# Kernel optimization log

Measured on AMD Instinct MI355X. Metric: run time of the kernel, lower is better.

Reference implementation:

```python
import jax, jax.numpy as jnp
import numpy as np

B, T, U, L, C = 2048, 100, 512, 3, 10


def setup_inputs() -> dict:
    key = jax.random.key(0)
    ks = jax.random.split(key, 2 + 3 * L + 2)
    x = jax.random.normal(ks[0], (B, T, 1), dtype=jnp.float32)
    mask = jax.random.randint(ks[1], (B, T), 0, 2) > 0
    inp = {"x": x, "mask": mask}
    in_dim = 1
    s = 2
    for l in range(L):
        # Keras LSTM kernel layout: gates ordered [i, f, g(candidate), o]
        inp[f"W{l}"] = jax.random.normal(ks[s], (in_dim, 4 * U), dtype=jnp.float32) * 0.05
        inp[f"U{l}"] = jax.random.normal(ks[s + 1], (U, 4 * U), dtype=jnp.float32) * 0.05
        b = np.zeros((4 * U,), dtype=np.float32)
        b[U:2 * U] = 1.0  # unit_forget_bias (Keras default)
        inp[f"b{l}"] = jnp.asarray(b)
        in_dim = U
        s += 2
    inp["Wd"] = jax.random.normal(ks[s], (U, C), dtype=jnp.float32) * 0.05
    inp["bd"] = jnp.zeros((C,), dtype=jnp.float32)
    return inp


def _lstm_step(x_t, h, c, W, Uw, b):
    z = x_t @ W + h @ Uw + b  # [B, 4U]
    i, f, g, o = jnp.split(z, 4, axis=-1)
    i = jax.nn.sigmoid(i)
    f = jax.nn.sigmoid(f)
    g = jnp.tanh(g)
    o = jax.nn.sigmoid(o)
    c_new = f * c + i * g
    h_new = o * jnp.tanh(c_new)
    return h_new, c_new


def reference(x, mask, W0, U0, b0, W1, U1, b1, W2, U2, b2, Wd, bd):
    params = [(W0, U0, b0), (W1, U1, b1), (W2, U2, b2)]
    xt = jnp.swapaxes(x, 0, 1)        # [T, B, 1]
    mt = jnp.swapaxes(mask, 0, 1)     # [T, B]
    Bsz = x.shape[0]
    init = tuple((jnp.zeros((Bsz, U), x.dtype), jnp.zeros((Bsz, U), x.dtype)) for _ in range(L))

    def scan_fn(carry, inp_t):
        x_t, m_t = inp_t
        m = m_t[:, None]  # [B, 1]
        new_states = []
        layer_in = x_t
        for (h, c), (W, Uw, b) in zip(carry, params):
            h_new, c_new = _lstm_step(layer_in, h, c, W, Uw, b)
            # Keras mask semantics: masked steps carry state/output forward
            h_new = jnp.where(m, h_new, h)
            c_new = jnp.where(m, c_new, c)
            new_states.append((h_new, c_new))
            layer_in = h_new
        return tuple(new_states), None

    final, _ = jax.lax.scan(scan_fn, init, (xt, mt))
    h_top = final[-1][0]  # [B, U]
    logits = h_top @ Wd + bd
    return jax.nn.softmax(logits, axis=-1)
```

## Files before the change

### kernel.cpp

```cpp
#include <hip/hip_runtime.h>
#include <cstdint>
#include <cstddef>

#define B_   2048
#define T_   100
#define U_   512
#define NG_  2048
#define C_   10

typedef __attribute__((ext_vector_type(8))) short   short8;
typedef __attribute__((ext_vector_type(4))) float   floatx4;
typedef unsigned short ushort_t;

__device__ inline ushort_t f2bf(float f){
  unsigned u = __float_as_uint(f);
  unsigned r = (u + 0x7FFFu + ((u >> 16) & 1u)) >> 16;
  return (ushort_t)r;
}
__device__ inline float bf2f(ushort_t b){ return __uint_as_float(((unsigned)b) << 16); }

__device__ inline float sigm(float x){ return 1.0f / (1.0f + __expf(-x)); }
__device__ inline float tanh_fast(float x){
  float a = fabsf(x);
  float e = __expf(-2.0f * a);
  float r = (1.0f - e) / (1.0f + e);
  return copysignf(r, x);
}

__device__ inline int orig_col(int p){
  int Tt  = p >> 7;
  int loc = p & 127;
  int half = loc >> 6;
  int loc2 = loc & 63;
  int gate = loc2 >> 4;
  int uu   = (half << 4) | (loc2 & 15);
  return gate * U_ + Tt * 32 + uu;
}

#define AS1(p) ((const __attribute__((address_space(1))) void*)(p))
#define AS3(p) ((__attribute__((address_space(3))) void*)(p))

__global__ void convert_weights(
    const float* __restrict__ W0, const float* __restrict__ U0, const float* __restrict__ b0,
    const float* __restrict__ W1, const float* __restrict__ U1, const float* __restrict__ b1,
    const float* __restrict__ W2, const float* __restrict__ U2, const float* __restrict__ b2,
    ushort_t* __restrict__ Bt0, ushort_t* __restrict__ Bt1, ushort_t* __restrict__ Bt2,
    float* __restrict__ W0p, float* __restrict__ biasp)
{
  const int N0 = NG_ * 512;
  const int N1 = NG_ * 1024;
  const int total = N0 + 2 * N1 + NG_ + 3 * NG_;
  int idx = blockIdx.x * 256 + threadIdx.x;
  if (idx >= total) return;

  if (idx < N0){
    int p = idx >> 9, k = idx & 511;
    Bt0[idx] = f2bf(U0[(size_t)k * NG_ + orig_col(p)]);
  } else if (idx < N0 + N1){
    int j = idx - N0; int p = j >> 10, k = j & 1023;
    int oc = orig_col(p);
    float v = (k < 512) ? W1[(size_t)k * NG_ + oc] : U1[(size_t)(k - 512) * NG_ + oc];
    Bt1[j] = f2bf(v);
  } else if (idx < N0 + 2 * N1){
    int j = idx - N0 - N1; int p = j >> 10, k = j & 1023;
    int oc = orig_col(p);
    float v = (k < 512) ? W2[(size_t)k * NG_ + oc] : U2[(size_t)(k - 512) * NG_ + oc];
    Bt2[j] = f2bf(v);
  } else if (idx < N0 + 2 * N1 + NG_){
    int p = idx - N0 - 2 * N1;
    W0p[p] = W0[orig_col(p)];
  } else {
    int j = idx - N0 - 2 * N1 - NG_;
    int l = j >> 11, p = j & 2047;
    const float* bs = (l == 0) ? b0 : (l == 1) ? b1 : b2;
    biasp[j] = bs[orig_col(p)];
  }
}

template<int LAYER>
__device__ __forceinline__ void do_task(
    const ushort_t* __restrict__ A0,
    const ushort_t* __restrict__ A1,
    const ushort_t* __restrict__ Bt,
    const float* __restrict__ biasp,
    const float* __restrict__ W0p,
    const float* __restrict__ x,
    const int* __restrict__ mask,
    float* __restrict__ cbuf,
    const ushort_t* __restrict__ hprev,
    ushort_t* __restrict__ hout,
    int t, int mt, int nt,
    ushort_t* tA, ushort_t* tB)
{
  constexpr int NPHASE = (LAYER == 0) ? 1 : 2;
  constexpr bool IS_L0 = (LAYER == 0);
  constexpr int K = NPHASE * 512;

  const int tid  = threadIdx.x;
  const int wv   = tid >> 6;
  const int lane = tid & 63;
  const int qd   = lane >> 4;
  const int l16  = lane & 15;
  const int wave_m = wv >> 1;
  const int wave_n = wv & 1;
  const int m0 = mt * 128, n0 = nt * 128;

  int srow[4], scol[4];
  #pragma unroll
  for (int cc2 = 0; cc2 < 4; ++cc2){
    int i = cc2 * 256 + wv * 64 + lane;
    srow[cc2] = i >> 3;
    scol[cc2] = ((i & 7) + (i >> 3)) & 7;
  }

  int aoff[2][4], boff[2][4];
  #pragma unroll
  for (int ks = 0; ks < 2; ++ks){
    #pragma unroll
    for (int w = 0; w < 4; ++w){
      int Ra = wave_m * 64 + w * 16 + l16;
      int Rb = wave_n * 64 + w * 16 + l16;
      int q  = ks * 4 + qd;
      aoff[ks][w] = Ra * 64 + ((q - Ra) & 7) * 8;
      boff[ks][w] = Rb * 64 + ((q - Rb) & 7) * 8;
    }
  }

  floatx4 acc[4][4];
  #pragma unroll
  for (int i = 0; i < 4; ++i)
    #pragma unroll
    for (int j = 0; j < 4; ++j) acc[i][j] = (floatx4){0.f, 0.f, 0.f, 0.f};

  #pragma unroll
  for (int ph = 0; ph < NPHASE; ++ph){
    const ushort_t* A = (NPHASE == 2 && ph == 1) ? A1 : A0;
    for (int k0 = 0; k0 < 512; k0 += 64){
      #pragma unroll
      for (int cc2 = 0; cc2 < 4; ++cc2){
        int ibase = cc2 * 256 + wv * 64;
        const ushort_t* ga = A + (size_t)(m0 + srow[cc2]) * U_ + k0 + scol[cc2] * 8;
        __builtin_amdgcn_global_load_lds(AS1(ga), AS3(&tA[ibase * 8]), 16, 0, 0);
        const ushort_t* gb = Bt + (size_t)(n0 + srow[cc2]) * K + ph * 512 + k0 + scol[cc2] * 8;
        __builtin_amdgcn_global_load_lds(AS1(gb), AS3(&tB[ibase * 8]), 16, 0, 0);
      }
      __syncthreads();

      #pragma unroll
      for (int ks = 0; ks < 2; ++ks){
        short8 af[4], bfr[4];
        #pragma unroll
        for (int wm = 0; wm < 4; ++wm)
          af[wm] = *(const short8*)&tA[aoff[ks][wm]];
        #pragma unroll
        for (int wn = 0; wn < 4; ++wn)
          bfr[wn] = *(const short8*)&tB[boff[ks][wn]];
        #pragma unroll
        for (int wm = 0; wm < 4; ++wm)
          #pragma unroll
          for (int wn = 0; wn < 4; ++wn)
            acc[wm][wn] = __builtin_amdgcn_mfma_f32_16x16x32_bf16(af[wm], bfr[wn], acc[wm][wn], 0, 0, 0);
      }
      __syncthreads();
    }
  }

  const int u  = nt * 32 + wave_n * 16 + l16;
  const int pb = nt * 128 + wave_n * 64 + l16;
  const float bi = biasp[pb], bf_ = biasp[pb + 16], bg = biasp[pb + 32], bo = biasp[pb + 48];
  float wi = 0.f, wf = 0.f, wg = 0.f, wo = 0.f;
  if (IS_L0){ wi = W0p[pb]; wf = W0p[pb + 16]; wg = W0p[pb + 32]; wo = W0p[pb + 48]; }

  #pragma unroll
  for (int wm = 0; wm < 4; ++wm){
    #pragma unroll
    for (int reg = 0; reg < 4; ++reg){
      int b = m0 + wave_m * 64 + wm * 16 + qd * 4 + reg;
      float zi = acc[wm][0][reg] + bi;
      float zf = acc[wm][1][reg] + bf_;
      float zg = acc[wm][2][reg] + bg;
      float zo = acc[wm][3][reg] + bo;
      if (IS_L0){
        float xv = x[(size_t)b * T_ + t];
        zi += xv * wi; zf += xv * wf; zg += xv * wg; zo += xv * wo;
      }
      int mk = mask[(size_t)b * T_ + t];
      size_t su = (size_t)b * U_ + u;
      float c_old = cbuf[su];
      float i_ = sigm(zi), f_ = sigm(zf), g_ = tanh_fast(zg), o_ = sigm(zo);
      float c_new = f_ * c_old + i_ * g_;
      float h_new = o_ * tanh_fast(c_new);
      ushort_t hb = mk ? f2bf(h_new) : hprev[su];
      cbuf[su] = mk ? c_new : c_old;
      hout[su] = hb;
    }
  }
}

__global__ __launch_bounds__(256, 3) void lstm_phase(
    const ushort_t* __restrict__ Bt0, const ushort_t* __restrict__ Bt1,
    const ushort_t* __restrict__ Bt2, const float* __restrict__ biasp,
    const float* __restrict__ W0p, const float* __restrict__ x,
    const int* __restrict__ mask,
    ushort_t* h00, ushort_t* h01, ushort_t* h10, ushort_t* h11,
    ushort_t* h20, ushort_t* h21,
    float* c0, float* c1, float* c2,
    int s)
{
  __shared__ __align__(16) ushort_t tA[128 * 64];
  __shared__ __align__(16) ushort_t tB[128 * 64];

  const int lin  = blockIdx.x;
  const int task = lin >> 8;
  const int tile = lin & 255;
  const int mt = tile >> 4, nt = tile & 15;

  ushort_t* h0[2] = {h00, h01};
  ushort_t* h1[2] = {h10, h11};
  ushort_t* h2[2] = {h20, h21};

  if (task == 0){
    if (s >= 100) return;
    int t = s, p = t & 1;
    do_task<0>(h0[p], nullptr, Bt0, biasp, W0p, x, mask,
               c0, h0[p], h0[p ^ 1], t, mt, nt, tA, tB);
  } else if (task == 1){
    if (s < 1 || s > 100) return;
    int t = s - 1, p = t & 1;
    do_task<1>(h0[p ^ 1], h1[p], Bt1, biasp + NG_, nullptr, x, mask,
               c1, h1[p], h1[p ^ 1], t, mt, nt, tA, tB);
  } else {
    if (s < 2) return;
    int t = s - 2, p = t & 1;
    do_task<2>(h1[p ^ 1], h2[p], Bt2, biasp + 2 * NG_, nullptr, x, mask,
               c2, h2[p], h2[p ^ 1], t, mt, nt, tA, tB);
  }
}

__global__ __launch_bounds__(256) void head_softmax(
    const ushort_t* __restrict__ h2, const float* __restrict__ Wd,
    const float* __restrict__ bd, float* __restrict__ out)
{
  int wv = threadIdx.x >> 6, lane = threadIdx.x & 63;
  int row = blockIdx.x * 4 + wv;
  const ushort_t* hr = h2 + (size_t)row * U_;

  float acc[C_];
  #pragma unroll
  for (int c = 0; c < C_; ++c) acc[c] = 0.f;

  short8 hv = *(const short8*)&hr[lane * 8];
  #pragma unroll
  for (int j = 0; j < 8; ++j){
    float hf = bf2f((ushort_t)hv[j]);
    int k = lane * 8 + j;
    #pragma unroll
    for (int c = 0; c < C_; ++c) acc[c] += hf * Wd[k * C_ + c];
  }
  #pragma unroll
  for (int c = 0; c < C_; ++c){
    float v = acc[c];
    #pragma unroll
    for (int off = 32; off > 0; off >>= 1) v += __shfl_xor(v, off);
    acc[c] = v + bd[c];
  }
  float mx = acc[0];
  #pragma unroll
  for (int c = 1; c < C_; ++c) mx = fmaxf(mx, acc[c]);
  float e[C_]; float s = 0.f;
  #pragma unroll
  for (int c = 0; c < C_; ++c){ e[c] = __expf(acc[c] - mx); s += e[c]; }
  float inv = 1.0f / s;
  if (lane == 0){
    #pragma unroll
    for (int c = 0; c < C_; ++c) out[(size_t)row * C_ + c] = e[c] * inv;
  }
}

extern "C" void kernel_launch(void* const* d_in, const int* in_sizes, int n_in,
                              void* d_out, int out_size, void* d_ws, size_t ws_size,
                              hipStream_t stream)
{
  const float* x  = (const float*)d_in[0];
  const int*  mask= (const int*)  d_in[1];
  const float* W0 = (const float*)d_in[2];
  const float* U0 = (const float*)d_in[3];
  const float* b0 = (const float*)d_in[4];
  const float* W1 = (const float*)d_in[5];
  const float* U1 = (const float*)d_in[6];
  const float* b1 = (const float*)d_in[7];
  const float* W2 = (const float*)d_in[8];
  const float* U2 = (const float*)d_in[9];
  const float* b2 = (const float*)d_in[10];
  const float* Wd = (const float*)d_in[11];
  const float* bd = (const float*)d_in[12];
  float* out = (float*)d_out;

  char* ws = (char*)d_ws;
  size_t off = 0;
  auto alloc = [&](size_t sz) -> char* {
    char* p = ws + off; off = (off + sz + 255) & ~(size_t)255; return p;
  };
  ushort_t* Bt0  = (ushort_t*)alloc((size_t)NG_ * 512 * 2);
  ushort_t* Bt1  = (ushort_t*)alloc((size_t)NG_ * 1024 * 2);
  ushort_t* Bt2  = (ushort_t*)alloc((size_t)NG_ * 1024 * 2);
  float*    W0p  = (float*)alloc((size_t)NG_ * 4);
  float*    biasp= (float*)alloc((size_t)3 * NG_ * 4);

  const size_t hsz = (size_t)B_ * U_ * 2;
  const size_t csz = (size_t)B_ * U_ * 4;
  char* state = alloc(6 * hsz + 3 * csz);
  ushort_t* hb[3][2]; float* cb[3];
  {
    char* pp = state;
    for (int l = 0; l < 3; ++l)
      for (int par = 0; par < 2; ++par){ hb[l][par] = (ushort_t*)pp; pp += hsz; }
    for (int l = 0; l < 3; ++l){ cb[l] = (float*)pp; pp += csz; }
  }

  hipMemsetAsync(state, 0, 6 * hsz + 3 * csz, stream);

  const int total = NG_ * 512 + 2 * NG_ * 1024 + NG_ + 3 * NG_;
  convert_weights<<<(total + 255) / 256, 256, 0, stream>>>(
      W0, U0, b0, W1, U1, b1, W2, U2, b2, Bt0, Bt1, Bt2, W0p, biasp);

  for (int s = 0; s < 102; ++s){
    lstm_phase<<<768, 256, 0, stream>>>(
        Bt0, Bt1, Bt2, biasp, W0p, x, mask,
        hb[0][0], hb[0][1], hb[1][0], hb[1][1], hb[2][0], hb[2][1],
        cb[0], cb[1], cb[2], s);
  }

  head_softmax<<<B_ / 4, 256, 0, stream>>>(hb[2][0], Wd, bd, out);
}
```

Baseline: 3.425 ms.

## Store hidden state in MFMA fragment layout and double-buffer B tiles

The hidden-state buffers are rewritten in a blocked 16-row by 8-column layout, so each lane can load its A fragments for the MFMA directly from global memory without first staging them in LDS. Only the weight tile B is staged through LDS now, and it is double-buffered so the next k-slice loads while the current one computes, which removes one barrier per iteration. The head kernel is updated to read the new layout. The cost is A fragments coming straight from global/L2 with no reuse across the two N-waves, which may increase global traffic.

```diff
diff --git a/kernel.cpp b/kernel.cpp
--- a/kernel.cpp
+++ b/kernel.cpp
@@ -7,6 +7,7 @@
 #define U_   512
 #define NG_  2048
 #define C_   10
+
 
 typedef __attribute__((ext_vector_type(8))) short   short8;
 typedef __attribute__((ext_vector_type(4))) float   floatx4;
@@ -35,6 +36,10 @@
   int gate = loc2 >> 4;
   int uu   = (half << 4) | (loc2 & 15);
   return gate * U_ + Tt * 32 + uu;
+}
+
+__device__ inline size_t hidx(int b, int u){
+  return (((size_t)(b >> 4) * 64 + (size_t)(u >> 3)) * 16 + (b & 15)) * 8 + (u & 7);
 }
 
 #define AS1(p) ((const __attribute__((address_space(1))) void*)(p))
@@ -90,11 +95,12 @@
     const ushort_t* __restrict__ hprev,
     ushort_t* __restrict__ hout,
     int t, int mt, int nt,
-    ushort_t* tA, ushort_t* tB)
+    ushort_t* tB)
 {
   constexpr int NPHASE = (LAYER == 0) ? 1 : 2;
   constexpr bool IS_L0 = (LAYER == 0);
-  constexpr int K = NPHASE * 512;
+  constexpr int K  = NPHASE * 512;
+  constexpr int NK = NPHASE * 8;
 
   const int tid  = threadIdx.x;
   const int wv   = tid >> 6;
@@ -107,62 +113,79 @@
 
   int srow[4], scol[4];
   #pragma unroll
-  for (int cc2 = 0; cc2 < 4; ++cc2){
-    int i = cc2 * 256 + wv * 64 + lane;
-    srow[cc2] = i >> 3;
-    scol[cc2] = ((i & 7) + (i >> 3)) & 7;
-  }
-
-  int aoff[2][4], boff[2][4];
+  for (int cc = 0; cc < 4; ++cc){
+    int i = cc * 256 + tid;
+    srow[cc] = i >> 3;
+    scol[cc] = ((i & 7) + (i >> 3)) & 7;
+  }
+
+  int boff[2][4];
   #pragma unroll
   for (int ks = 0; ks < 2; ++ks){
     #pragma unroll
     for (int w = 0; w < 4; ++w){
-      int Ra = wave_m * 64 + w * 16 + l16;
       int Rb = wave_n * 64 + w * 16 + l16;
       int q  = ks * 4 + qd;
-      aoff[ks][w] = Ra * 64 + ((q - Ra) & 7) * 8;
       boff[ks][w] = Rb * 64 + ((q - Rb) & 7) * 8;
     }
   }
 
+  size_t abase[4];
+  #pragma unroll
+  for (int wm = 0; wm < 4; ++wm)
+    abase[wm] = ((size_t)((m0 >> 4) + wave_m * 4 + wm)) * 8192
+              + (size_t)qd * 128 + (size_t)l16 * 8;
+
   floatx4 acc[4][4];
   #pragma unroll
   for (int i = 0; i < 4; ++i)
     #pragma unroll
     for (int j = 0; j < 4; ++j) acc[i][j] = (floatx4){0.f, 0.f, 0.f, 0.f};
 
-  #pragma unroll
-  for (int ph = 0; ph < NPHASE; ++ph){
-    const ushort_t* A = (NPHASE == 2 && ph == 1) ? A1 : A0;
-    for (int k0 = 0; k0 < 512; k0 += 64){
+  auto stageB = [&](int kk, int buf){
+    const int phh = kk >> 3;
+    const int kk0 = (kk & 7) << 6;
+    ushort_t* dst = tB + buf * 8192;
+    #pragma unroll
+    for (int cc = 0; cc < 4; ++cc){
+      const int ibase = cc * 256 + wv * 64;
+      const ushort_t* gb = Bt + (size_t)(n0 + srow[cc]) * K + phh * 512 + kk0 + scol[cc] * 8;
+      __builtin_amdgcn_global_load_lds(AS1(gb), AS3(&dst[ibase * 8]), 16, 0, 0);
+    }
+  };
+
+  stageB(0, 0);
+  __syncthreads();
+
+  int cur = 0;
+  for (int kk = 0; kk < NK; ++kk){
+    const int k0 = (kk & 7) << 6;
+    const ushort_t* A = (NPHASE == 2 && kk >= 8) ? A1 : A0;
+
+    short8 af[2][4];
+    #pragma unroll
+    for (int ks = 0; ks < 2; ++ks)
       #pragma unroll
-      for (int cc2 = 0; cc2 < 4; ++cc2){
-        int ibase = cc2 * 256 + wv * 64;
-        const ushort_t* ga = A + (size_t)(m0 + srow[cc2]) * U_ + k0 + scol[cc2] * 8;
-        __builtin_amdgcn_global_load_lds(AS1(ga), AS3(&tA[ibase * 8]), 16, 0, 0);
-        const ushort_t* gb = Bt + (size_t)(n0 + srow[cc2]) * K + ph * 512 + k0 + scol[cc2] * 8;
-        __builtin_amdgcn_global_load_lds(AS1(gb), AS3(&tB[ibase * 8]), 16, 0, 0);
-      }
-      __syncthreads();
-
+      for (int wm = 0; wm < 4; ++wm)
+        af[ks][wm] = *(const short8*)&A[abase[wm] + (size_t)(k0 * 16 + ks * 512)];
+
+    if (kk + 1 < NK) stageB(kk + 1, cur ^ 1);
+
+    const ushort_t* tb = tB + cur * 8192;
+    #pragma unroll
+    for (int ks = 0; ks < 2; ++ks){
+      short8 bfr[4];
       #pragma unroll
-      for (int ks = 0; ks < 2; ++ks){
-        short8 af[4], bfr[4];
-        #pragma unroll
-        for (int wm = 0; wm < 4; ++wm)
-          af[wm] = *(const short8*)&tA[aoff[ks][wm]];
+      for (int wn = 0; wn < 4; ++wn)
+        bfr[wn] = *(const short8*)&tb[boff[ks][wn]];
+      #pragma unroll
+      for (int wm = 0; wm < 4; ++wm)
         #pragma unroll
         for (int wn = 0; wn < 4; ++wn)
-          bfr[wn] = *(const short8*)&tB[boff[ks][wn]];
-        #pragma unroll
-        for (int wm = 0; wm < 4; ++wm)
-          #pragma unroll
-          for (int wn = 0; wn < 4; ++wn)
-            acc[wm][wn] = __builtin_amdgcn_mfma_f32_16x16x32_bf16(af[wm], bfr[wn], acc[wm][wn], 0, 0, 0);
-      }
-      __syncthreads();
+          acc[wm][wn] = __builtin_amdgcn_mfma_f32_16x16x32_bf16(af[ks][wm], bfr[wn], acc[wm][wn], 0, 0, 0);
     }
+    __syncthreads();
+    cur ^= 1;
   }
 
   const int u  = nt * 32 + wave_n * 16 + l16;
@@ -186,13 +209,14 @@
       }
       int mk = mask[(size_t)b * T_ + t];
       size_t su = (size_t)b * U_ + u;
+      size_t sf = hidx(b, u);
       float c_old = cbuf[su];
       float i_ = sigm(zi), f_ = sigm(zf), g_ = tanh_fast(zg), o_ = sigm(zo);
       float c_new = f_ * c_old + i_ * g_;
       float h_new = o_ * tanh_fast(c_new);
-      ushort_t hb = mk ? f2bf(h_new) : hprev[su];
+      ushort_t hb = mk ? f2bf(h_new) : hprev[sf];
       cbuf[su] = mk ? c_new : c_old;
-      hout[su] = hb;
+      hout[sf] = hb;
     }
   }
 }
@@ -207,8 +231,7 @@
     float* c0, float* c1, float* c2,
     int s)
 {
-  __shared__ __align__(16) ushort_t tA[128 * 64];
-  __shared__ __align__(16) ushort_t tB[128 * 64];
+  __shared__ __align__(16) ushort_t tB[2 * 128 * 64];
 
   const int lin  = blockIdx.x;
   const int task = lin >> 8;
@@ -223,17 +246,17 @@
     if (s >= 100) return;
     int t = s, p = t & 1;
     do_task<0>(h0[p], nullptr, Bt0, biasp, W0p, x, mask,
-               c0, h0[p], h0[p ^ 1], t, mt, nt, tA, tB);
+               c0, h0[p], h0[p ^ 1], t, mt, nt, tB);
   } else if (task == 1){
     if (s < 1 || s > 100) return;
     int t = s - 1, p = t & 1;
     do_task<1>(h0[p ^ 1], h1[p], Bt1, biasp + NG_, nullptr, x, mask,
-               c1, h1[p], h1[p ^ 1], t, mt, nt, tA, tB);
+               c1, h1[p], h1[p ^ 1], t, mt, nt, tB);
   } else {
     if (s < 2) return;
     int t = s - 2, p = t & 1;
     do_task<2>(h1[p ^ 1], h2[p], Bt2, biasp + 2 * NG_, nullptr, x, mask,
-               c2, h2[p], h2[p ^ 1], t, mt, nt, tA, tB);
+               c2, h2[p], h2[p ^ 1], t, mt, nt, tB);
   }
 }
 
@@ -243,13 +266,13 @@
 {
   int wv = threadIdx.x >> 6, lane = threadIdx.x & 63;
   int row = blockIdx.x * 4 + wv;
-  const ushort_t* hr = h2 + (size_t)row * U_;
+  const ushort_t* hr = h2 + (((size_t)(row >> 4) * 64 + lane) * 16 + (row & 15)) * 8;
 
   float acc[C_];
   #pragma unroll
   for (int c = 0; c < C_; ++c) acc[c] = 0.f;
 
-  short8 hv = *(const short8*)&hr[lane * 8];
+  short8 hv = *(const short8*)hr;
   #pragma unroll
   for (int j = 0; j < 8; ++j){
     float hf = bf2f((ushort_t)hv[j]);
```

Result: slower. 4.146 ms (+21.0%).

## Triple-buffer LDS tiles with async prefetch two K-steps ahead in LSTM GEMM

Applied to the files above, without the earlier changes.

Replaces the single-buffered K=64 tile loop, which used two __syncthreads per step, with a three-stage ring of K=32 LDS tiles. Global-to-LDS loads are issued two steps ahead and guarded by explicit vmcnt waits and one barrier per step. The goal is to overlap global memory latency with MFMA work inside each recurrent step. In exchange it adds more barriers overall because the K-steps are smaller, uses a new swizzle for the narrower tiles, and relies on hand-tuned waitcnt values whose correctness depends on how many loads are in flight.

```diff
diff --git a/kernel.cpp b/kernel.cpp
--- a/kernel.cpp
+++ b/kernel.cpp
@@ -7,6 +7,7 @@
 #define U_   512
 #define NG_  2048
 #define C_   10
+
 
 typedef __attribute__((ext_vector_type(8))) short   short8;
 typedef __attribute__((ext_vector_type(4))) float   floatx4;
@@ -94,7 +95,8 @@
 {
   constexpr int NPHASE = (LAYER == 0) ? 1 : 2;
   constexpr bool IS_L0 = (LAYER == 0);
-  constexpr int K = NPHASE * 512;
+  constexpr int K  = NPHASE * 512;
+  constexpr int NK = NPHASE * 16;
 
   const int tid  = threadIdx.x;
   const int wv   = tid >> 6;
@@ -105,64 +107,73 @@
   const int wave_n = wv & 1;
   const int m0 = mt * 128, n0 = nt * 128;
 
-  int srow[4], scol[4];
-  #pragma unroll
-  for (int cc2 = 0; cc2 < 4; ++cc2){
-    int i = cc2 * 256 + wv * 64 + lane;
-    srow[cc2] = i >> 3;
-    scol[cc2] = ((i & 7) + (i >> 3)) & 7;
-  }
-
-  int aoff[2][4], boff[2][4];
-  #pragma unroll
-  for (int ks = 0; ks < 2; ++ks){
-    #pragma unroll
-    for (int w = 0; w < 4; ++w){
-      int Ra = wave_m * 64 + w * 16 + l16;
-      int Rb = wave_n * 64 + w * 16 + l16;
-      int q  = ks * 4 + qd;
-      aoff[ks][w] = Ra * 64 + ((q - Ra) & 7) * 8;
-      boff[ks][w] = Rb * 64 + ((q - Rb) & 7) * 8;
+  int srow[2], scol[2];
+  #pragma unroll
+  for (int cc = 0; cc < 2; ++cc){
+    int i = cc * 256 + tid;
+    srow[cc] = i >> 2;
+    scol[cc] = ((i & 3) + ((i >> 2) >> 1)) & 3;
+  }
+
+  int aoff[4], boff[4];
+  #pragma unroll
+  for (int w = 0; w < 4; ++w){
+    int Ra = wave_m * 64 + w * 16 + l16;
+    int Rb = wave_n * 64 + w * 16 + l16;
+    aoff[w] = Ra * 32 + ((qd - (Ra >> 1)) & 3) * 8;
+    boff[w] = Rb * 32 + ((qd - (Rb >> 1)) & 3) * 8;
+  }
+
+  floatx4 acc[4][4];
+  #pragma unroll
+  for (int i = 0; i < 4; ++i)
+    #pragma unroll
+    for (int j = 0; j < 4; ++j) acc[i][j] = (floatx4){0.f, 0.f, 0.f, 0.f};
+
+  auto stage = [&](int kk, int b){
+    const ushort_t* A = (NPHASE == 2 && kk >= 16) ? A1 : A0;
+    const int kk0 = (kk & 15) << 5;
+    ushort_t* dA = tA + b * 4096;
+    ushort_t* dB = tB + b * 4096;
+    #pragma unroll
+    for (int cc = 0; cc < 2; ++cc){
+      const int ibase = cc * 256 + wv * 64;
+      const ushort_t* ga = A + (size_t)(m0 + srow[cc]) * U_ + kk0 + scol[cc] * 8;
+      __builtin_amdgcn_global_load_lds(AS1(ga), AS3(&dA[ibase * 8]), 16, 0, 0);
+      const ushort_t* gb = Bt + (size_t)(n0 + srow[cc]) * K + kk * 32 + scol[cc] * 8;
+      __builtin_amdgcn_global_load_lds(AS1(gb), AS3(&dB[ibase * 8]), 16, 0, 0);
     }
-  }
-
-  floatx4 acc[4][4];
-  #pragma unroll
-  for (int i = 0; i < 4; ++i)
-    #pragma unroll
-    for (int j = 0; j < 4; ++j) acc[i][j] = (floatx4){0.f, 0.f, 0.f, 0.f};
-
-  #pragma unroll
-  for (int ph = 0; ph < NPHASE; ++ph){
-    const ushort_t* A = (NPHASE == 2 && ph == 1) ? A1 : A0;
-    for (int k0 = 0; k0 < 512; k0 += 64){
+  };
+
+  stage(0, 0);
+  stage(1, 1);
+  asm volatile("s_waitcnt vmcnt(4)" ::: "memory");
+  __builtin_amdgcn_s_barrier();
+  __builtin_amdgcn_sched_barrier(0);
+
+  #pragma unroll
+  for (int kk = 0; kk < NK; ++kk){
+    const int buf = kk % 3;
+
+    if (kk + 2 < NK) stage(kk + 2, (kk + 2) % 3);
+
+    const ushort_t* ta = tA + buf * 4096;
+    const ushort_t* tb = tB + buf * 4096;
+    short8 af[4], bfr[4];
+    #pragma unroll
+    for (int w = 0; w < 4; ++w) af[w]  = *(const short8*)&ta[aoff[w]];
+    #pragma unroll
+    for (int w = 0; w < 4; ++w) bfr[w] = *(const short8*)&tb[boff[w]];
+    #pragma unroll
+    for (int wm = 0; wm < 4; ++wm)
       #pragma unroll
-      for (int cc2 = 0; cc2 < 4; ++cc2){
-        int ibase = cc2 * 256 + wv * 64;
-        const ushort_t* ga = A + (size_t)(m0 + srow[cc2]) * U_ + k0 + scol[cc2] * 8;
-        __builtin_amdgcn_global_load_lds(AS1(ga), AS3(&tA[ibase * 8]), 16, 0, 0);
-        const ushort_t* gb = Bt + (size_t)(n0 + srow[cc2]) * K + ph * 512 + k0 + scol[cc2] * 8;
-        __builtin_amdgcn_global_load_lds(AS1(gb), AS3(&tB[ibase * 8]), 16, 0, 0);
-      }
-      __syncthreads();
-
-      #pragma unroll
-      for (int ks = 0; ks < 2; ++ks){
-        short8 af[4], bfr[4];
-        #pragma unroll
-        for (int wm = 0; wm < 4; ++wm)
-          af[wm] = *(const short8*)&tA[aoff[ks][wm]];
-        #pragma unroll
-        for (int wn = 0; wn < 4; ++wn)
-          bfr[wn] = *(const short8*)&tB[boff[ks][wn]];
-        #pragma unroll
-        for (int wm = 0; wm < 4; ++wm)
-          #pragma unroll
-          for (int wn = 0; wn < 4; ++wn)
-            acc[wm][wn] = __builtin_amdgcn_mfma_f32_16x16x32_bf16(af[wm], bfr[wn], acc[wm][wn], 0, 0, 0);
-      }
-      __syncthreads();
-    }
+      for (int wn = 0; wn < 4; ++wn)
+        acc[wm][wn] = __builtin_amdgcn_mfma_f32_16x16x32_bf16(af[wm], bfr[wn], acc[wm][wn], 0, 0, 0);
+
+    if (kk + 2 < NK) asm volatile("s_waitcnt vmcnt(4) lgkmcnt(0)" ::: "memory");
+    else             asm volatile("s_waitcnt vmcnt(0) lgkmcnt(0)" ::: "memory");
+    __builtin_amdgcn_s_barrier();
+    __builtin_amdgcn_sched_barrier(0);
   }
 
   const int u  = nt * 32 + wave_n * 16 + l16;
@@ -207,8 +218,8 @@
     float* c0, float* c1, float* c2,
     int s)
 {
-  __shared__ __align__(16) ushort_t tA[128 * 64];
-  __shared__ __align__(16) ushort_t tB[128 * 64];
+  __shared__ __align__(16) ushort_t tA[3 * 128 * 32];
+  __shared__ __align__(16) ushort_t tB[3 * 128 * 32];
 
   const int lin  = blockIdx.x;
   const int task = lin >> 8;
```

Result: slower. 4.046 ms (+18.1%).

## Enlarge LSTM GEMM tiles to 256x256 with 512-thread blocks

Applied to the files above, without the earlier changes.

Each workgroup now computes a 256x256 output tile using 8 waves (2x4), each holding 8x4 MFMA accumulators, instead of 128x128 with 4 waves. The grid shrinks from 768 to 192 blocks per step, and the weight column permutation changes to match the wider N tile. The aim is more operand reuse per LDS load and fewer global loads of A and B. In exchange, only 192 blocks run on a GPU with many more CUs (and fewer on edge steps where some tasks exit), and register pressure rises from the doubled accumulator count.

```diff
diff --git a/kernel.cpp b/kernel.cpp
--- a/kernel.cpp
+++ b/kernel.cpp
@@ -7,6 +7,7 @@
 #define U_   512
 #define NG_  2048
 #define C_   10
+
 
 typedef __attribute__((ext_vector_type(8))) short   short8;
 typedef __attribute__((ext_vector_type(4))) float   floatx4;
@@ -28,13 +29,13 @@
 }
 
 __device__ inline int orig_col(int p){
-  int Tt  = p >> 7;
-  int loc = p & 127;
-  int half = loc >> 6;
+  int Tt   = p >> 8;
+  int loc  = p & 255;
+  int wn   = loc >> 6;
   int loc2 = loc & 63;
   int gate = loc2 >> 4;
-  int uu   = (half << 4) | (loc2 & 15);
-  return gate * U_ + Tt * 32 + uu;
+  int uu   = loc2 & 15;
+  return gate * U_ + Tt * 64 + wn * 16 + uu;
 }
 
 #define AS1(p) ((const __attribute__((address_space(1))) void*)(p))
@@ -101,34 +102,38 @@
   const int lane = tid & 63;
   const int qd   = lane >> 4;
   const int l16  = lane & 15;
-  const int wave_m = wv >> 1;
-  const int wave_n = wv & 1;
-  const int m0 = mt * 128, n0 = nt * 128;
+  const int wave_m = wv >> 2;
+  const int wave_n = wv & 3;
+  const int m0 = mt * 256, n0 = nt * 256;
 
   int srow[4], scol[4];
   #pragma unroll
-  for (int cc2 = 0; cc2 < 4; ++cc2){
-    int i = cc2 * 256 + wv * 64 + lane;
-    srow[cc2] = i >> 3;
-    scol[cc2] = ((i & 7) + (i >> 3)) & 7;
-  }
-
-  int aoff[2][4], boff[2][4];
+  for (int cc = 0; cc < 4; ++cc){
+    int i = cc * 512 + tid;
+    srow[cc] = i >> 3;
+    scol[cc] = ((i & 7) + (i >> 3)) & 7;
+  }
+
+  int aoff[2][8], boff[2][4];
   #pragma unroll
   for (int ks = 0; ks < 2; ++ks){
     #pragma unroll
+    for (int w = 0; w < 8; ++w){
+      int Ra = wave_m * 128 + w * 16 + l16;
+      int q  = ks * 4 + qd;
+      aoff[ks][w] = Ra * 64 + ((q - Ra) & 7) * 8;
+    }
+    #pragma unroll
     for (int w = 0; w < 4; ++w){
-      int Ra = wave_m * 64 + w * 16 + l16;
       int Rb = wave_n * 64 + w * 16 + l16;
       int q  = ks * 4 + qd;
-      aoff[ks][w] = Ra * 64 + ((q - Ra) & 7) * 8;
       boff[ks][w] = Rb * 64 + ((q - Rb) & 7) * 8;
     }
   }
 
-  floatx4 acc[4][4];
-  #pragma unroll
-  for (int i = 0; i < 4; ++i)
+  floatx4 acc[8][4];
+  #pragma unroll
+  for (int i = 0; i < 8; ++i)
     #pragma unroll
     for (int j = 0; j < 4; ++j) acc[i][j] = (floatx4){0.f, 0.f, 0.f, 0.f};
 
@@ -137,26 +142,26 @@
     const ushort_t* A = (NPHASE == 2 && ph == 1) ? A1 : A0;
     for (int k0 = 0; k0 < 512; k0 += 64){
       #pragma unroll
-      for (int cc2 = 0; cc2 < 4; ++cc2){
-        int ibase = cc2 * 256 + wv * 64;
-        const ushort_t* ga = A + (size_t)(m0 + srow[cc2]) * U_ + k0 + scol[cc2] * 8;
+      for (int cc = 0; cc < 4; ++cc){
+        int ibase = cc * 512 + wv * 64;
+        const ushort_t* ga = A + (size_t)(m0 + srow[cc]) * U_ + k0 + scol[cc] * 8;
         __builtin_amdgcn_global_load_lds(AS1(ga), AS3(&tA[ibase * 8]), 16, 0, 0);
-        const ushort_t* gb = Bt + (size_t)(n0 + srow[cc2]) * K + ph * 512 + k0 + scol[cc2] * 8;
+        const ushort_t* gb = Bt + (size_t)(n0 + srow[cc]) * K + ph * 512 + k0 + scol[cc] * 8;
         __builtin_amdgcn_global_load_lds(AS1(gb), AS3(&tB[ibase * 8]), 16, 0, 0);
       }
       __syncthreads();
 
       #pragma unroll
       for (int ks = 0; ks < 2; ++ks){
-        short8 af[4], bfr[4];
+        short8 af[8], bfr[4];
         #pragma unroll
-        for (int wm = 0; wm < 4; ++wm)
-          af[wm] = *(const short8*)&tA[aoff[ks][wm]];
+        for (int w = 0; w < 8; ++w)
+          af[w] = *(const short8*)&tA[aoff[ks][w]];
         #pragma unroll
-        for (int wn = 0; wn < 4; ++wn)
-          bfr[wn] = *(const short8*)&tB[boff[ks][wn]];
+        for (int w = 0; w < 4; ++w)
+          bfr[w] = *(const short8*)&tB[boff[ks][w]];
         #pragma unroll
-        for (int wm = 0; wm < 4; ++wm)
+        for (int wm = 0; wm < 8; ++wm)
           #pragma unroll
           for (int wn = 0; wn < 4; ++wn)
             acc[wm][wn] = __builtin_amdgcn_mfma_f32_16x16x32_bf16(af[wm], bfr[wn], acc[wm][wn], 0, 0, 0);
@@ -165,17 +170,17 @@
     }
   }
 
-  const int u  = nt * 32 + wave_n * 16 + l16;
-  const int pb = nt * 128 + wave_n * 64 + l16;
+  const int u  = nt * 64 + wave_n * 16 + l16;
+  const int pb = nt * 256 + wave_n * 64 + l16;
   const float bi = biasp[pb], bf_ = biasp[pb + 16], bg = biasp[pb + 32], bo = biasp[pb + 48];
   float wi = 0.f, wf = 0.f, wg = 0.f, wo = 0.f;
   if (IS_L0){ wi = W0p[pb]; wf = W0p[pb + 16]; wg = W0p[pb + 32]; wo = W0p[pb + 48]; }
 
   #pragma unroll
-  for (int wm = 0; wm < 4; ++wm){
+  for (int wm = 0; wm < 8; ++wm){
     #pragma unroll
     for (int reg = 0; reg < 4; ++reg){
-      int b = m0 + wave_m * 64 + wm * 16 + qd * 4 + reg;
+      int b = m0 + wave_m * 128 + wm * 16 + qd * 4 + reg;
       float zi = acc[wm][0][reg] + bi;
       float zf = acc[wm][1][reg] + bf_;
       float zg = acc[wm][2][reg] + bg;
@@ -197,7 +202,7 @@
   }
 }
 
-__global__ __launch_bounds__(256, 3) void lstm_phase(
+__global__ __launch_bounds__(512, 2) void lstm_phase(
     const ushort_t* __restrict__ Bt0, const ushort_t* __restrict__ Bt1,
     const ushort_t* __restrict__ Bt2, const float* __restrict__ biasp,
     const float* __restrict__ W0p, const float* __restrict__ x,
@@ -207,13 +212,13 @@
     float* c0, float* c1, float* c2,
     int s)
 {
-  __shared__ __align__(16) ushort_t tA[128 * 64];
-  __shared__ __align__(16) ushort_t tB[128 * 64];
+  __shared__ __align__(16) ushort_t tA[256 * 64];
+  __shared__ __align__(16) ushort_t tB[256 * 64];
 
   const int lin  = blockIdx.x;
-  const int task = lin >> 8;
-  const int tile = lin & 255;
-  const int mt = tile >> 4, nt = tile & 15;
+  const int task = lin >> 6;
+  const int tile = lin & 63;
+  const int mt = tile >> 3, nt = tile & 7;
 
   ushort_t* h0[2] = {h00, h01};
   ushort_t* h1[2] = {h10, h11};
@@ -325,7 +330,7 @@
       W0, U0, b0, W1, U1, b1, W2, U2, b2, Bt0, Bt1, Bt2, W0p, biasp);
 
   for (int s = 0; s < 102; ++s){
-    lstm_phase<<<768, 256, 0, stream>>>(
+    lstm_phase<<<192, 512, 0, stream>>>(
         Bt0, Bt1, Bt2, biasp, W0p, x, mask,
         hb[0][0], hb[0][1], hb[1][0], hb[1][1], hb[2][0], hb[2][1],
         cb[0], cb[1], cb[2], s);
```

New measurement: 6.965 ms. +103.3%, slower.
